# Optimization experiments

Measured on AMD Instinct MI355X. Metric: run time of the kernel, lower is better.

Reference implementation:

```python
import jax, jax.numpy as jnp
import numpy as np

R_MAX = 10000.0  # eval_para['r_max']
L_MAX = 1        # eval_para['l_max']


def _mlp(energy, W1, b1, W2, b2, W3, b3):
    h = jax.nn.relu(energy @ W1 + b1)
    h = jax.nn.relu(h @ W2 + b2)
    return h @ W3 + b3


def _dsc_eigs(ptl):
    rn = ptl.shape[0]
    r = jnp.linspace(R_MAX / rn, R_MAX, rn).astype(ptl.dtype)  # radial grid
    l = jnp.arange(L_MAX + 1, dtype=ptl.dtype)[:, None]        # [L+1, 1]
    # H = -lap/2 + diag(ptl) + l(l+1) diag(1/r^2)
    # -(-2*I)/2 contributes +1 on the diagonal; off-diagonals are -1/2.
    diag = 1.0 + ptl[None, :] + l * (l + 1) / (r * r)[None, :]  # [L+1, rn]
    idx = jnp.arange(rn)
    H = jnp.zeros((L_MAX + 1, rn, rn), dtype=ptl.dtype)
    H = H.at[:, idx, idx].set(diag)
    i = jnp.arange(rn - 1)
    H = H.at[:, i, i + 1].set(-0.5).at[:, i + 1, i].set(-0.5)
    return jnp.linalg.eigvalsh(H)  # [L+1, rn], ascending eigenvalues


def setup_inputs() -> dict:
    key = jax.random.key(0)
    k = jax.random.split(key, 4)
    CLIP, H1, H2, RN = 4096, 2048, 1024, 4096
    energy = jax.random.normal(k[0], (CLIP,), dtype=jnp.float32)
    W1 = jax.random.normal(k[1], (CLIP, H1), dtype=jnp.float32) / np.sqrt(CLIP)
    W2 = jax.random.normal(k[2], (H1, H2), dtype=jnp.float32) / np.sqrt(H1)
    W3 = jax.random.normal(k[3], (H2, RN), dtype=jnp.float32) / np.sqrt(H2)
    return {
        'energy': energy,
        'W1': W1, 'b1': jnp.zeros((H1,), jnp.float32),
        'W2': W2, 'b2': jnp.zeros((H2,), jnp.float32),
        'W3': W3, 'b3': jnp.zeros((RN,), jnp.float32),
    }


def reference(energy, W1, b1, W2, b2, W3, b3):
    ptl_md = _mlp(energy, W1, b1, W2, b2, W3, b3)  # [rn] predicted potential
    evl_md = _dsc_eigs(ptl_md)                     # [L_MAX+1, rn] eigenvalues
    return (ptl_md, evl_md)
```

## Files before the change

kernel.cpp:

```cpp
#include <hip/hip_runtime.h>

#define CLIP 4096
#define H1   2048
#define H2   1024
#define RN   4096
#define H_STEP 2.44140625f
#define G1   32768

__device__ __forceinline__ unsigned fmap(float f) {
    unsigned u = __float_as_uint(f);
    return (u & 0x80000000u) ? ~u : (u | 0x80000000u);
}
__device__ __forceinline__ float funmap(unsigned u) {
    return __uint_as_float((u & 0x80000000u) ? (u & 0x7fffffffu) : ~u);
}
__device__ __forceinline__ void spect_bounds(const unsigned* bu, float& lo, float& cell) {
    float mn = funmap(bu[0]), mx = funmap(bu[1]);
    lo = mn - 1e-3f;
    float hi = mx + 2.33554432f + 1e-3f;
    cell = (hi - lo) * (1.0f / (float)G1);
}

__global__ __launch_bounds__(256) void part1(const float* __restrict__ W,
                                             const float* __restrict__ x,
                                             float* __restrict__ partA,
                                             unsigned* __restrict__ bu) {
    if (blockIdx.x == 0 && blockIdx.y == 0 && threadIdx.x == 0) {
        bu[0] = 0xFFFFFFFFu;
        bu[1] = 0u;
    }
    int j = blockIdx.x * 256 + threadIdx.x;
    int i0 = blockIdx.y * 64;
    const float* Wp = W + (size_t)i0 * H1 + j;
    float acc = 0.f;
#pragma unroll 8
    for (int i = 0; i < 64; ++i)
        acc = fmaf(x[i0 + i], Wp[(size_t)i * H1], acc);
    partA[(size_t)blockIdx.y * H1 + j] = acc;
}

__global__ __launch_bounds__(256) void part2f(const float* __restrict__ W,
                                              const float* __restrict__ partA,
                                              const float* __restrict__ b,
                                              float* __restrict__ partB) {
    __shared__ float xs[16];
    int t = threadIdx.x;
    int i_loc = t >> 4, c_loc = t & 15;
    int i0 = blockIdx.y * 16;
    float s = 0.f;
#pragma unroll
    for (int k = 0; k < 4; ++k)
        s += partA[(size_t)(c_loc + 16 * k) * H1 + i0 + i_loc];
    s += __shfl_xor(s, 1); s += __shfl_xor(s, 2);
    s += __shfl_xor(s, 4); s += __shfl_xor(s, 8);
    if (c_loc == 0) xs[i_loc] = fmaxf(s + b[i0 + i_loc], 0.f);
    __syncthreads();
    float xv[16];
#pragma unroll
    for (int u = 0; u < 16; ++u) xv[u] = xs[u];
    int j = blockIdx.x * 256 + t;
    const float* Wp = W + (size_t)i0 * H2 + j;
    float acc = 0.f;
#pragma unroll
    for (int i = 0; i < 16; ++i)
        acc = fmaf(xv[i], Wp[(size_t)i * H2], acc);
    partB[(size_t)blockIdx.y * H2 + j] = acc;
}

__global__ __launch_bounds__(256) void part3f(const float* __restrict__ W,
                                              const float* __restrict__ partB,
                                              const float* __restrict__ b,
                                              float* __restrict__ partA) {
    __shared__ float xs[32];
    int t = threadIdx.x;
    int i_loc = t >> 3, c_loc = t & 7;
    int i0 = blockIdx.y * 32;
    float s = 0.f;
#pragma unroll
    for (int k = 0; k < 16; ++k)
        s += partB[(size_t)(c_loc + 8 * k) * H2 + i0 + i_loc];
    s += __shfl_xor(s, 1); s += __shfl_xor(s, 2); s += __shfl_xor(s, 4);
    if (c_loc == 0) xs[i_loc] = fmaxf(s + b[i0 + i_loc], 0.f);
    __syncthreads();
    float xv[32];
#pragma unroll
    for (int u = 0; u < 32; ++u) xv[u] = xs[u];
    int j = blockIdx.x * 256 + t;
    const float* Wp = W + (size_t)i0 * RN + j;
    float acc = 0.f;
#pragma unroll
    for (int i = 0; i < 32; ++i)
        acc = fmaf(xv[i], Wp[(size_t)i * RN], acc);
    partA[(size_t)blockIdx.y * RN + j] = acc;
}

__global__ __launch_bounds__(256) void fin3(const float* __restrict__ partA,
                                            const float* __restrict__ b,
                                            float* __restrict__ out,
                                            float* __restrict__ D,
                                            unsigned* __restrict__ bu) {
    __shared__ float smn[4], smx[4];
    int j = blockIdx.x * 256 + threadIdx.x;
    float s = b[j];
#pragma unroll 8
    for (int c = 0; c < 32; ++c) s += partA[(size_t)c * RN + j];
    out[j] = s;
    float r = H_STEP * (float)(j + 1);
    float base = 2.0f + 2.0f * s;
    D[j] = base;
    D[RN + j] = base + 4.0f / (r * r);
    float mn = s, mx = s;
    for (int off = 32; off; off >>= 1) {
        mn = fminf(mn, __shfl_down(mn, off));
        mx = fmaxf(mx, __shfl_down(mx, off));
    }
    int tid = threadIdx.x;
    if ((tid & 63) == 0) { smn[tid >> 6] = mn; smx[tid >> 6] = mx; }
    __syncthreads();
    if (tid == 0) {
        for (int w = 1; w < 4; ++w) { mn = fminf(mn, smn[w]); mx = fmaxf(mx, smx[w]); }
        atomicMin(&bu[0], fmap(mn));
        atomicMax(&bu[1], fmap(mx));
    }
}

#define STEP_B(dv)                                                         \
    {                                                                      \
        float tt = (dv) - X;                                               \
        float p = fmaf(tt, pm1, pm2);                                      \
        r = __builtin_amdgcn_alignbit(r, __float_as_uint(p), 31);          \
        pm2 = pm1; pm1 = p;                                                \
    }
#define STEP_A(dv)                                                         \
    {                                                                      \
        float tt = X - (dv);                                               \
        float p = fmaf(tt, pm1, pm2);                                      \
        r = __builtin_amdgcn_alignbit(r, __float_as_uint(p), 31);          \
        pm2 = pm1; pm1 = p;                                                \
    }
#define CNT16                                                              \
    {                                                                      \
        unsigned xx = ((r ^ (r >> 1)) ^ 0x5555u) & 0xFFFFu;                \
        cnt += (unsigned)__builtin_popcount(xx);                           \
    }
#define RENORM                                                             \
    {                                                                      \
        unsigned a1 = __float_as_uint(pm1) & 0x7fffffffu;                  \
        unsigned a2 = __float_as_uint(pm2) & 0x7fffffffu;                  \
        unsigned hm = a1 > a2 ? a1 : a2;                                   \
        int es = 254 - (int)(hm >> 23);                                    \
        es = es < 1 ? 1 : es;                                              \
        float sc = __uint_as_float((unsigned)es << 23);                    \
        pm1 *= sc; pm2 *= sc;                                              \
    }
#define GRP16(v0, v1, v2, v3)                                              \
    {                                                                      \
        STEP_B(v0.x) STEP_A(v0.y) STEP_B(v0.z) STEP_A(v0.w)                \
        STEP_B(v1.x) STEP_A(v1.y) STEP_B(v1.z) STEP_A(v1.w)                \
        STEP_B(v2.x) STEP_A(v2.y) STEP_B(v2.z) STEP_A(v2.w)                \
        STEP_B(v3.x) STEP_A(v3.y) STEP_B(v3.z) STEP_A(v3.w)                \
        CNT16                                                              \
        RENORM                                                             \
    }
#define GRP16R(q3, q2, q1, q0)                                             \
    {                                                                      \
        STEP_B(q3.w) STEP_A(q3.z) STEP_B(q3.y) STEP_A(q3.x)                \
        STEP_B(q2.w) STEP_A(q2.z) STEP_B(q2.y) STEP_A(q2.x)                \
        STEP_B(q1.w) STEP_A(q1.z) STEP_B(q1.y) STEP_A(q1.x)                \
        STEP_B(q0.w) STEP_A(q0.z) STEP_B(q0.y) STEP_A(q0.x)                \
        CNT16                                                              \
        RENORM                                                             \
    }

__global__ __launch_bounds__(256) void stage1(const float* __restrict__ Dall,
                                              const unsigned* __restrict__ bu,
                                              int* __restrict__ counts) {
    __shared__ alignas(16) float ds[RN];
    __shared__ float shB1[128], shB2[128];
    __shared__ int   shCB[128];
    const int t = threadIdx.x, l = blockIdx.y;
    const float* Dsrc = Dall + (l << 12);
    for (int i = t; i < RN / 4; i += 256)
        reinterpret_cast<float4*>(ds)[i] = reinterpret_cast<const float4*>(Dsrc)[i];
    __syncthreads();

    float lo, cell;
    spect_bounds(bu, lo, cell);
    int xi = t & 127, dir = t >> 7;
    int j = blockIdx.x * 128 + xi;
    float X = 2.0f * (lo + cell * (float)j);

    float pm1 = 1.0f, pm2 = 0.0f;
    unsigned cnt = 0, r = 0;
    const float4* d4 = reinterpret_cast<const float4*>(ds);

    if (dir == 0) {
#pragma unroll 4
        for (int g = 0; g < 128; ++g) {
            float4 a = d4[4 * g], b2 = d4[4 * g + 1];
            float4 c2 = d4[4 * g + 2], e2 = d4[4 * g + 3];
            GRP16(a, b2, c2, e2)
        }
    } else {
#pragma unroll 4
        for (int g = 0; g < 127; ++g) {
            int base = 1020 - 4 * g;
            float4 a3 = d4[base + 3], a2 = d4[base + 2];
            float4 a1 = d4[base + 1], a0 = d4[base];
            GRP16R(a3, a2, a1, a0)
        }
        {
            float4 a = d4[515], b2 = d4[514], c2 = d4[513], e2 = d4[512];
            STEP_B(a.w)  STEP_A(a.z)  STEP_B(a.y)  STEP_A(a.x)
            STEP_B(b2.w) STEP_A(b2.z) STEP_B(b2.y) STEP_A(b2.x)
            STEP_B(c2.w) STEP_A(c2.z) STEP_B(c2.y) STEP_A(c2.x)
            STEP_B(e2.w) STEP_A(e2.z) STEP_B(e2.y)
            unsigned xx = ((r ^ (r >> 1)) ^ 0x2AAAu) & 0x7FFFu;
            cnt += (unsigned)__builtin_popcount(xx);
        }
        shB1[xi] = pm1; shB2[xi] = pm2; shCB[xi] = (int)cnt;
    }
    __syncthreads();
    if (dir == 0) {
        float u1 = pm1, u2 = pm2;
        float w1 = shB1[xi], w2 = shB2[xi];
        float Dm = ds[2048];
        float gg = -(Dm - X) * u1 * w1 - u2 * w1 + u1 * w2;
        unsigned sx = (__float_as_uint(gg) ^ __float_as_uint(u1) ^
                       __float_as_uint(w1)) >> 31;
        counts[(l << 15) + j] = (int)(cnt + (unsigned)shCB[xi] + (sx ^ 1u));
    }
}

__global__ __launch_bounds__(256) void final_eig(const int* __restrict__ counts,
                                                 const unsigned* __restrict__ bu,
                                                 float* __restrict__ out) {
    int e = blockIdx.x * 256 + threadIdx.x;
    int l = e >> 12, k = e & (RN - 1);
    const int* c = counts + (l << 15);
    int lo_i = 0, hi_i = G1 - 1;
    while (lo_i < hi_i) {
        int mid = (lo_i + hi_i + 1) >> 1;
        if (c[mid] <= k) lo_i = mid; else hi_i = mid - 1;
    }
    while (lo_i > 0 && c[lo_i] > k) --lo_i;
    while (lo_i < G1 - 1 && c[lo_i + 1] <= k) ++lo_i;
    float lo, cell;
    spect_bounds(bu, lo, cell);
    out[e] = lo + cell * ((float)lo_i + 0.5f);
}

extern "C" void kernel_launch(void* const* d_in, const int* in_sizes, int n_in,
                              void* d_out, int out_size, void* d_ws, size_t ws_size,
                              hipStream_t stream) {
    const float* energy = (const float*)d_in[0];
    const float* W1 = (const float*)d_in[1];
    const float* b1 = (const float*)d_in[2];
    const float* W2 = (const float*)d_in[3];
    const float* b2 = (const float*)d_in[4];
    const float* W3 = (const float*)d_in[5];
    const float* b3 = (const float*)d_in[6];
    float* out = (float*)d_out;

    float* ws = (float*)d_ws;
    float*    partA  = ws;
    float*    partB  = partA + 131072;
    float*    D      = partB + 131072;
    unsigned* bu     = (unsigned*)(D + 2 * RN);
    int*      counts = (int*)(bu + 4);

    part1 <<<dim3(8, 64),  256, 0, stream>>>(W1, energy, partA, bu);
    part2f<<<dim3(4, 128), 256, 0, stream>>>(W2, partA, b1, partB);
    part3f<<<dim3(16, 32), 256, 0, stream>>>(W3, partB, b2, partA);
    fin3  <<<RN / 256,     256, 0, stream>>>(partA, b3, out, D, bu);

    stage1<<<dim3(G1 / 128, 2), 256, 0, stream>>>(D, bu, counts);
    final_eig<<<2 * RN / 256, 256, 0, stream>>>(counts, bu, out + RN);
}
```

Baseline: 58.57 us.

## Vectorize MLP GEMV loads with float4 and rebalance split-K partitioning

```diff
diff --git a/kernel.cpp b/kernel.cpp
--- a/kernel.cpp
+++ b/kernel.cpp
@@ -29,69 +29,86 @@
         bu[0] = 0xFFFFFFFFu;
         bu[1] = 0u;
     }
-    int j = blockIdx.x * 256 + threadIdx.x;
-    int i0 = blockIdx.y * 64;
-    const float* Wp = W + (size_t)i0 * H1 + j;
-    float acc = 0.f;
-#pragma unroll 8
-    for (int i = 0; i < 64; ++i)
-        acc = fmaf(x[i0 + i], Wp[(size_t)i * H1], acc);
-    partA[(size_t)blockIdx.y * H1 + j] = acc;
+    int j4 = (blockIdx.x * 256 + threadIdx.x) << 2;
+    int i0 = blockIdx.y * 16;
+    const float* Wp = W + (size_t)i0 * H1 + j4;
+    float4 acc = make_float4(0.f, 0.f, 0.f, 0.f);
+#pragma unroll
+    for (int i = 0; i < 16; ++i) {
+        float xi = x[i0 + i];
+        float4 w = *reinterpret_cast<const float4*>(Wp + (size_t)i * H1);
+        acc.x = fmaf(xi, w.x, acc.x);
+        acc.y = fmaf(xi, w.y, acc.y);
+        acc.z = fmaf(xi, w.z, acc.z);
+        acc.w = fmaf(xi, w.w, acc.w);
+    }
+    *reinterpret_cast<float4*>(partA + (size_t)blockIdx.y * H1 + j4) = acc;
 }
 
 __global__ __launch_bounds__(256) void part2f(const float* __restrict__ W,
                                               const float* __restrict__ partA,
                                               const float* __restrict__ b,
                                               float* __restrict__ partB) {
-    __shared__ float xs[16];
+    __shared__ float xs[8];
     int t = threadIdx.x;
-    int i_loc = t >> 4, c_loc = t & 15;
-    int i0 = blockIdx.y * 16;
+    int i_loc = t >> 5, lane = t & 31;
+    int i0 = blockIdx.y * 8;
     float s = 0.f;
 #pragma unroll
-    for (int k = 0; k < 4; ++k)
-        s += partA[(size_t)(c_loc + 16 * k) * H1 + i0 + i_loc];
-    s += __shfl_xor(s, 1); s += __shfl_xor(s, 2);
-    s += __shfl_xor(s, 4); s += __shfl_xor(s, 8);
-    if (c_loc == 0) xs[i_loc] = fmaxf(s + b[i0 + i_loc], 0.f);
-    __syncthreads();
-    float xv[16];
-#pragma unroll
-    for (int u = 0; u < 16; ++u) xv[u] = xs[u];
-    int j = blockIdx.x * 256 + t;
-    const float* Wp = W + (size_t)i0 * H2 + j;
-    float acc = 0.f;
-#pragma unroll
-    for (int i = 0; i < 16; ++i)
-        acc = fmaf(xv[i], Wp[(size_t)i * H2], acc);
-    partB[(size_t)blockIdx.y * H2 + j] = acc;
+    for (int k = 0; k < 8; ++k)
+        s += partA[(size_t)(lane + 32 * k) * H1 + i0 + i_loc];
+    s += __shfl_xor(s, 1); s += __shfl_xor(s, 2); s += __shfl_xor(s, 4);
+    s += __shfl_xor(s, 8); s += __shfl_xor(s, 16);
+    if (lane == 0) xs[i_loc] = fmaxf(s + b[i0 + i_loc], 0.f);
+    __syncthreads();
+    float xv[8];
+#pragma unroll
+    for (int u = 0; u < 8; ++u) xv[u] = xs[u];
+    int j4 = t << 2;
+    const float* Wp = W + (size_t)i0 * H2 + j4;
+    float4 acc = make_float4(0.f, 0.f, 0.f, 0.f);
+#pragma unroll
+    for (int i = 0; i < 8; ++i) {
+        float4 w = *reinterpret_cast<const float4*>(Wp + (size_t)i * H2);
+        acc.x = fmaf(xv[i], w.x, acc.x);
+        acc.y = fmaf(xv[i], w.y, acc.y);
+        acc.z = fmaf(xv[i], w.z, acc.z);
+        acc.w = fmaf(xv[i], w.w, acc.w);
+    }
+    *reinterpret_cast<float4*>(partB + (size_t)blockIdx.y * H2 + j4) = acc;
 }
 
 __global__ __launch_bounds__(256) void part3f(const float* __restrict__ W,
                                               const float* __restrict__ partB,
                                               const float* __restrict__ b,
                                               float* __restrict__ partA) {
-    __shared__ float xs[32];
+    __shared__ float xs[8];
     int t = threadIdx.x;
-    int i_loc = t >> 3, c_loc = t & 7;
-    int i0 = blockIdx.y * 32;
+    int i_loc = t >> 5, lane = t & 31;
+    int i0 = blockIdx.y * 8;
     float s = 0.f;
 #pragma unroll
-    for (int k = 0; k < 16; ++k)
-        s += partB[(size_t)(c_loc + 8 * k) * H2 + i0 + i_loc];
+    for (int k = 0; k < 8; ++k)
+        s += partB[(size_t)(lane + 32 * k) * H2 + i0 + i_loc];
     s += __shfl_xor(s, 1); s += __shfl_xor(s, 2); s += __shfl_xor(s, 4);
-    if (c_loc == 0) xs[i_loc] = fmaxf(s + b[i0 + i_loc], 0.f);
-    __syncthreads();
-    float xv[32];
-#pragma unroll
-    for (int u = 0; u < 32; ++u) xv[u] = xs[u];
-    int j = blockIdx.x * 256 + t;
-    const float* Wp = W + (size_t)i0 * RN + j;
-    float acc = 0.f;
-#pragma unroll
-    for (int i = 0; i < 32; ++i)
-        acc = fmaf(xv[i], Wp[(size_t)i * RN], acc);
-    partA[(size_t)blockIdx.y * RN + j] = acc;
+    s += __shfl_xor(s, 8); s += __shfl_xor(s, 16);
+    if (lane == 0) xs[i_loc] = fmaxf(s + b[i0 + i_loc], 0.f);
+    __syncthreads();
+    float xv[8];
+#pragma unroll
+    for (int u = 0; u < 8; ++u) xv[u] = xs[u];
+    int j4 = (blockIdx.x * 256 + t) << 2;
+    const float* Wp = W + (size_t)i0 * RN + j4;
+    float4 acc = make_float4(0.f, 0.f, 0.f, 0.f);
+#pragma unroll
+    for (int i = 0; i < 8; ++i) {
+        float4 w = *reinterpret_cast<const float4*>(Wp + (size_t)i * RN);
+        acc.x = fmaf(xv[i], w.x, acc.x);
+        acc.y = fmaf(xv[i], w.y, acc.y);
+        acc.z = fmaf(xv[i], w.z, acc.z);
+        acc.w = fmaf(xv[i], w.w, acc.w);
+    }
+    *reinterpret_cast<float4*>(partA + (size_t)blockIdx.y * RN + j4) = acc;
 }
 
 __global__ __launch_bounds__(256) void fin3(const float* __restrict__ partA,
@@ -103,7 +120,7 @@
     int j = blockIdx.x * 256 + threadIdx.x;
     float s = b[j];
 #pragma unroll 8
-    for (int c = 0; c < 32; ++c) s += partA[(size_t)c * RN + j];
+    for (int c = 0; c < 128; ++c) s += partA[(size_t)c * RN + j];
     out[j] = s;
     float r = H_STEP * (float)(j + 1);
     float base = 2.0f + 2.0f * s;
@@ -264,14 +281,14 @@
 
     float* ws = (float*)d_ws;
     float*    partA  = ws;
-    float*    partB  = partA + 131072;
-    float*    D      = partB + 131072;
+    float*    partB  = partA + 524288;
+    float*    D      = partB + 262144;
     unsigned* bu     = (unsigned*)(D + 2 * RN);
     int*      counts = (int*)(bu + 4);
 
-    part1 <<<dim3(8, 64),  256, 0, stream>>>(W1, energy, partA, bu);
-    part2f<<<dim3(4, 128), 256, 0, stream>>>(W2, partA, b1, partB);
-    part3f<<<dim3(16, 32), 256, 0, stream>>>(W3, partB, b2, partA);
+    part1 <<<dim3(2, 256), 256, 0, stream>>>(W1, energy, partA, bu);
+    part2f<<<dim3(1, 256), 256, 0, stream>>>(W2, partA, b1, partB);
+    part3f<<<dim3(4, 128), 256, 0, stream>>>(W3, partB, b2, partA);
     fin3  <<<RN / 256,     256, 0, stream>>>(partA, b3, out, D, bu);
 
     stage1<<<dim3(G1 / 128, 2), 256, 0, stream>>>(D, bu, counts);
```

New measurement: 62.42 us. +6.6%, slower.
